# Performance work log

Measured on AMD Instinct MI355X. Metric: run time of the kernel, lower is better.

## Reference

```python
import jax, jax.numpy as jnp
import numpy as np

V = 28996  # BERT_VOCAB_SIZE
D = 768    # input_size (BERT embedding dim)
H = 768    # hidden_size
B, T, S = 32, 48, 128


def setup_inputs() -> dict:
    key = jax.random.key(0)
    ks = jax.random.split(key, 10)
    w = lambda k, shape: jax.random.normal(k, shape, jnp.float32) * 0.02
    return {
        "x": jax.random.normal(ks[0], (B, T, D), jnp.float32),
        "hidden_state": jax.random.normal(ks[1], (B, H), jnp.float32),
        "encoder_attention": jax.random.normal(ks[2], (B, S, H), jnp.float32),
        # GRUCell params (torch layout: weight_ih (3H, D), weight_hh (3H, H))
        "W_ih": w(ks[3], (3 * H, D)), "W_hh": w(ks[4], (3 * H, H)),
        "b_ih": jnp.zeros((3 * H,), jnp.float32), "b_hh": jnp.zeros((3 * H,), jnp.float32),
        # prediction_layer
        "W_pred": w(ks[5], (V, H)), "b_pred": jnp.zeros((V,), jnp.float32),
        # decoder_att_linear
        "W_att": w(ks[6], (H, H)), "b_att": jnp.zeros((H,), jnp.float32),
        # decoder_attn_weighted_ctx
        "W_ctx": w(ks[7], (H, 2 * H)), "b_ctx": jnp.zeros((H,), jnp.float32),
    }


def reference(x, hidden_state, encoder_attention,
              W_ih, W_hh, b_ih, b_hh,
              W_pred, b_pred, W_att, b_att, W_ctx, b_ctx):
    def gru(xt, h):  # torch nn.GRUCell math
        gi = xt @ W_ih.T + b_ih  # (B, 3H)
        gh = h @ W_hh.T + b_hh
        i_r, i_z, i_n = jnp.split(gi, 3, axis=-1)
        h_r, h_z, h_n = jnp.split(gh, 3, axis=-1)
        r = jax.nn.sigmoid(i_r + h_r)
        z = jax.nn.sigmoid(i_z + h_z)
        n = jnp.tanh(i_n + r * h_n)
        return (1.0 - z) * n + z * h

    def step(h, xt):  # xt: (B, D)
        h = gru(xt, h)
        logits = h @ W_pred.T + b_pred                      # (B, V)
        a = h @ W_att.T + b_att                              # (B, H)
        scores = jax.nn.softmax(
            jnp.einsum('bh,bsh->bs', a, encoder_attention), axis=-1)
        ctx = jnp.einsum('bs,bsh->bh', scores, encoder_attention)
        h_new = jnp.tanh(jnp.concatenate([ctx, h], axis=-1) @ W_ctx.T + b_ctx)
        return h_new, logits

    xT = jnp.swapaxes(x, 0, 1)  # (T, B, D)
    _, logits = jax.lax.scan(step, hidden_state, xT)  # logits: (T, B, V)
    return jnp.swapaxes(logits, 0, 1)  # (B, T, V)
```

## Files before the change

kernel.cpp:

```cpp
#include <hip/hip_runtime.h>
#include <hip/hip_bf16.h>

using bf16 = __hip_bfloat16;

typedef __attribute__((ext_vector_type(8))) short short8;
typedef __attribute__((ext_vector_type(4))) float floatx4;

#define BB 32
#define TT 48
#define SS 128
#define HH 768
#define VV 28996

__device__ __forceinline__ float sigmoidf_(float x) { return 1.0f / (1.0f + expf(-x)); }
__device__ __forceinline__ float tanhf_(float x) {
    float xx = fminf(fmaxf(x, -15.0f), 15.0f);
    float e = expf(2.0f * xx);
    return (e - 1.0f) / (e + 1.0f);
}

__device__ __forceinline__ float ld1cg(const float* p) {
    return __hip_atomic_load((float*)p, __ATOMIC_RELAXED, __HIP_MEMORY_SCOPE_AGENT);
}
__device__ __forceinline__ float2 ld2cg(const float* p) {
    unsigned long long u = __hip_atomic_load((unsigned long long*)p,
                                             __ATOMIC_RELAXED, __HIP_MEMORY_SCOPE_AGENT);
    union { unsigned long long u; float2 f; } c; c.u = u; return c.f;
}
__device__ __forceinline__ void st1cg(float* p, float v) {
    __hip_atomic_store(p, v, __ATOMIC_RELAXED, __HIP_MEMORY_SCOPE_AGENT);
}

__device__ __forceinline__ void split1(float v, bf16& h, bf16& l) {
    h = (bf16)v;
    l = (bf16)(v - __bfloat162float(h));
}

#define XQ    294912
#define WIHQ  442368
#define EQ    786432
#define WC1Q  147456
#define WATS  589824

__global__ __launch_bounds__(256)
void split_ops(const float* __restrict__ x, const float* __restrict__ Wih,
               const float* __restrict__ E, const float* __restrict__ Wctx,
               const float* __restrict__ Watt,
               bf16* __restrict__ xh, bf16* __restrict__ xl,
               bf16* __restrict__ wihh, bf16* __restrict__ wihl,
               bf16* __restrict__ eh, bf16* __restrict__ el,
               bf16* __restrict__ wc1h, bf16* __restrict__ wc1l,
               bf16* __restrict__ wath, bf16* __restrict__ watl)
{
    int idx = blockIdx.x * 256 + threadIdx.x;
    if (idx < XQ + WIHQ + EQ) {
        const float* src; bf16 *dh, *dl; int off;
        if (idx < XQ)            { src = x;   dh = xh;   dl = xl;   off = idx; }
        else if (idx < XQ + WIHQ){ src = Wih; dh = wihh; dl = wihl; off = idx - XQ; }
        else                     { src = E;   dh = eh;   dl = el;   off = idx - XQ - WIHQ; }
        float4 v = ((const float4*)src)[off];
        union { bf16 b[4]; uint2 u; } oh, ol;
        split1(v.x, oh.b[0], ol.b[0]); split1(v.y, oh.b[1], ol.b[1]);
        split1(v.z, oh.b[2], ol.b[2]); split1(v.w, oh.b[3], ol.b[3]);
        ((uint2*)dh)[off] = oh.u; ((uint2*)dl)[off] = ol.u;
    } else if (idx < XQ + WIHQ + EQ + WC1Q) {
        int rem = idx - XQ - WIHQ - EQ;
        int j = rem / 192, c4 = rem - j * 192;
        float4 v = *(const float4*)(Wctx + (size_t)j * 1536 + 4 * c4);
        union { bf16 b[4]; uint2 u; } oh, ol;
        split1(v.x, oh.b[0], ol.b[0]); split1(v.y, oh.b[1], ol.b[1]);
        split1(v.z, oh.b[2], ol.b[2]); split1(v.w, oh.b[3], ol.b[3]);
        ((uint2*)wc1h)[rem] = oh.u; ((uint2*)wc1l)[rem] = ol.u;
    } else if (idx < XQ + WIHQ + EQ + WC1Q + WATS) {
        int rem = idx - XQ - WIHQ - EQ - WC1Q;
        int n = rem / 768, k = rem - n * 768;
        float v = Watt[(size_t)k * 768 + n];
        bf16 h, l; split1(v, h, l);
        wath[rem] = h; watl[rem] = l;
    }
}

__global__ __launch_bounds__(256)
void gbias_k(const float* __restrict__ E, const float* __restrict__ batt,
             float* __restrict__ gbias)
{
    int row = blockIdx.x * 4 + (threadIdx.x >> 6);
    int lane = threadIdx.x & 63;
    const float* er = E + (size_t)row * 768;
    float acc = 0.f;
#pragma unroll
    for (int i = 0; i < 12; ++i) acc += er[i * 64 + lane] * batt[i * 64 + lane];
#pragma unroll
    for (int d = 32; d > 0; d >>= 1) acc += __shfl_xor(acc, d);
    if (lane == 0) gbias[row] = acc;
}

#define WPQ 5567232
__global__ __launch_bounds__(256)
void conv_pred(const float* __restrict__ Wp, bf16* __restrict__ Wpb)
{
    int idx = blockIdx.x * 256 + threadIdx.x;
    if (idx >= WPQ) return;
    float4 v = ((const float4*)Wp)[idx];
    union { bf16 b[4]; uint2 u; } o;
    o.b[0] = (bf16)v.x; o.b[1] = (bf16)v.y; o.b[2] = (bf16)v.z; o.b[3] = (bf16)v.w;
    ((uint2*)Wpb)[idx] = o.u;
}

__global__ __launch_bounds__(256)
void gemm_split(const bf16* __restrict__ Ahi, const bf16* __restrict__ Alo, int lda,
                const bf16* __restrict__ Bhi, const bf16* __restrict__ Blo, int ldb,
                const float* __restrict__ bias,
                float* __restrict__ C, int ldc, int M, int N, int K)
{
    __shared__ __align__(16) char smem[65536];
    const int tid  = threadIdx.x;
    const int lane = tid & 63;
    const int widx = tid >> 6;
    const int wm = widx >> 1, wn = widx & 1;
    const int m0 = blockIdx.y * 128, n0 = blockIdx.x * 128;

    floatx4 acc[4][4];
    const floatx4 fzero = {0.f, 0.f, 0.f, 0.f};
#pragma unroll
    for (int i = 0; i < 4; ++i)
#pragma unroll
        for (int j = 0; j < 4; ++j) acc[i][j] = fzero;

    const int srow = tid >> 3, sslot = tid & 7;

    for (int kb = 0; kb < K; kb += 64) {
        __syncthreads();
        const bf16* mats[4] = {Ahi, Alo, Bhi, Blo};
#pragma unroll
        for (int mt = 0; mt < 4; ++mt) {
            const bf16* base = mats[mt];
            int ld   = (mt < 2) ? lda : ldb;
            int row0 = (mt < 2) ? m0 : n0;
#pragma unroll
            for (int r = 0; r < 4; ++r) {
                int row = r * 32 + srow;
                int c = sslot ^ (row & 7);
                const bf16* gp = base + (size_t)(row0 + row) * ld + kb + c * 8;
                char* lp = smem + mt * 16384 + r * 4096 + widx * 1024;
                __builtin_amdgcn_global_load_lds(
                    (const __attribute__((address_space(1))) void*)gp,
                    (__attribute__((address_space(3))) void*)lp, 16, 0, 0);
            }
        }
        __syncthreads();
#pragma unroll
        for (int kc = 0; kc < 2; ++kc) {
            short8 ah[4], al[4], bh[4], bl[4];
#pragma unroll
            for (int i = 0; i < 4; ++i) {
                int mrow = wm * 64 + i * 16 + (lane & 15);
                int nrow = wn * 64 + i * 16 + (lane & 15);
                int ca = kc * 4 + (lane >> 4);
                int sm = (ca ^ (mrow & 7)) * 16, sn = (ca ^ (nrow & 7)) * 16;
                ah[i] = *(const short8*)(smem +         mrow * 128 + sm);
                al[i] = *(const short8*)(smem + 16384 + mrow * 128 + sm);
                bh[i] = *(const short8*)(smem + 32768 + nrow * 128 + sn);
                bl[i] = *(const short8*)(smem + 49152 + nrow * 128 + sn);
            }
#pragma unroll
            for (int i = 0; i < 4; ++i)
#pragma unroll
                for (int j = 0; j < 4; ++j) {
                    acc[i][j] = __builtin_amdgcn_mfma_f32_16x16x32_bf16(ah[i], bh[j], acc[i][j], 0, 0, 0);
                    acc[i][j] = __builtin_amdgcn_mfma_f32_16x16x32_bf16(ah[i], bl[j], acc[i][j], 0, 0, 0);
                    acc[i][j] = __builtin_amdgcn_mfma_f32_16x16x32_bf16(al[i], bh[j], acc[i][j], 0, 0, 0);
                }
        }
    }
#pragma unroll
    for (int i = 0; i < 4; ++i) {
        int gm0 = m0 + wm * 64 + i * 16 + (lane >> 4) * 4;
#pragma unroll
        for (int j = 0; j < 4; ++j) {
            int gn = n0 + wn * 64 + j * 16 + (lane & 15);
            float bv = bias ? bias[gn] : 0.0f;
#pragma unroll
            for (int r2 = 0; r2 < 4; ++r2)
                C[(size_t)(gm0 + r2) * ldc + gn] = acc[i][j][r2] + bv;
        }
    }
}

__global__ __launch_bounds__(256)
void gemm_bt(const bf16* __restrict__ A, int lda,
             const bf16* __restrict__ Bm, int ldb,
             const float* __restrict__ bias,
             float* __restrict__ C, int ldc, int M, int N, int K)
{
    __shared__ __align__(16) char smem[32768];
    const int tid  = threadIdx.x;
    const int lane = tid & 63;
    const int widx = tid >> 6;
    const int wm = widx >> 1, wn = widx & 1;
    const int m0 = blockIdx.y * 128, n0 = blockIdx.x * 128;

    floatx4 acc[4][4];
    const floatx4 fzero = {0.f, 0.f, 0.f, 0.f};
#pragma unroll
    for (int i = 0; i < 4; ++i)
#pragma unroll
        for (int j = 0; j < 4; ++j) acc[i][j] = fzero;

    const int srow = tid >> 3, sslot = tid & 7;

    for (int kb = 0; kb < K; kb += 64) {
        __syncthreads();
#pragma unroll
        for (int r = 0; r < 4; ++r) {
            int mrow = r * 32 + srow;
            int c = sslot ^ (mrow & 7);
            const bf16* gp = A + (size_t)(m0 + mrow) * lda + kb + c * 8;
            char* lp = smem + r * 4096 + widx * 1024;
            __builtin_amdgcn_global_load_lds(
                (const __attribute__((address_space(1))) void*)gp,
                (__attribute__((address_space(3))) void*)lp, 16, 0, 0);
        }
#pragma unroll
        for (int r = 0; r < 4; ++r) {
            int nrow = r * 32 + srow;
            int gn = n0 + nrow; if (gn > N - 1) gn = N - 1;
            int c = sslot ^ (nrow & 7);
            const bf16* gp = Bm + (size_t)gn * ldb + kb + c * 8;
            char* lp = smem + 16384 + r * 4096 + widx * 1024;
            __builtin_amdgcn_global_load_lds(
                (const __attribute__((address_space(1))) void*)gp,
                (__attribute__((address_space(3))) void*)lp, 16, 0, 0);
        }
        __syncthreads();
#pragma unroll
        for (int kc = 0; kc < 2; ++kc) {
            short8 af[4], bfr[4];
#pragma unroll
            for (int i = 0; i < 4; ++i) {
                int mrow = wm * 64 + i * 16 + (lane & 15);
                int nrow = wn * 64 + i * 16 + (lane & 15);
                int ca = kc * 4 + (lane >> 4);
                af[i]  = *(const short8*)(smem +         mrow * 128 + ((ca ^ (mrow & 7)) * 16));
                bfr[i] = *(const short8*)(smem + 16384 + nrow * 128 + ((ca ^ (nrow & 7)) * 16));
            }
#pragma unroll
            for (int i = 0; i < 4; ++i)
#pragma unroll
                for (int j = 0; j < 4; ++j)
                    acc[i][j] = __builtin_amdgcn_mfma_f32_16x16x32_bf16(af[i], bfr[j], acc[i][j], 0, 0, 0);
        }
    }
#pragma unroll
    for (int i = 0; i < 4; ++i) {
        int gm0 = m0 + wm * 64 + i * 16 + (lane >> 4) * 4;
#pragma unroll
        for (int j = 0; j < 4; ++j) {
            int gn = n0 + wn * 64 + j * 16 + (lane & 15);
            if (gn < N) {
                float bv = bias ? bias[gn] : 0.0f;
#pragma unroll
                for (int r2 = 0; r2 < 4; ++r2)
                    C[(size_t)(gm0 + r2) * ldc + gn] = acc[i][j][r2] + bv;
            }
        }
    }
}

__global__ __launch_bounds__(256)
void transpose_f(const float* __restrict__ F, float* __restrict__ Ft)
{
    __shared__ float tile[32][33];
    int tx = threadIdx.x & 31, ty = threadIdx.x >> 5;
    int r0 = blockIdx.x << 5, j0 = blockIdx.y << 5;
#pragma unroll
    for (int i = 0; i < 4; ++i)
        tile[ty + 8 * i][tx] = F[(size_t)(r0 + ty + 8 * i) * 768 + j0 + tx];
    __syncthreads();
#pragma unroll
    for (int i = 0; i < 4; ++i)
        Ft[(size_t)(j0 + ty + 8 * i) * 4096 + r0 + tx] = tile[tx][ty + 8 * i];
}

#define NBLK 256
__device__ __forceinline__ void flag_barrier(unsigned int* flags, unsigned int target)
{
    __syncthreads();
    if (threadIdx.x == 0)
        __hip_atomic_store(&flags[blockIdx.x * 4], target,
                           __ATOMIC_RELAXED, __HIP_MEMORY_SCOPE_AGENT);
    if (threadIdx.x < NBLK) {
        while (__hip_atomic_load(&flags[threadIdx.x * 4], __ATOMIC_RELAXED,
                                 __HIP_MEMORY_SCOPE_AGENT) < target)
            __builtin_amdgcn_s_sleep(1);
    }
    __syncthreads();
}

__global__ __launch_bounds__(512)
void seq_coop(const float* __restrict__ gi,
              const float* __restrict__ G,
              const float* __restrict__ Ft,
              const float* __restrict__ gbias,
              const float* __restrict__ h0,
              const float* __restrict__ Whh,
              const float* __restrict__ Wctx,
              const float* __restrict__ bhh,
              const float* __restrict__ bctx,
              float* __restrict__ Ha,
              float* __restrict__ Hb,
              float* __restrict__ Sc,
              unsigned int* __restrict__ flags,
              bf16* __restrict__ Hseq)
{
    const int bid  = blockIdx.x;
    const int tid  = threadIdx.x;
    const int w    = tid >> 6;
    const int lane = tid & 63;
    const int kg   = lane & 7;
    const int bo   = lane >> 3;
    const int j0   = bid * 3;

    __shared__ __align__(16) float Wlds[12][768];
    __shared__ float part[8][9][32];
    __shared__ float redsum[9][32];
    __shared__ float c2s[3][32];
    __shared__ float pT[128][33];
    __shared__ float ctxp[3][4][32];

    for (int idx = tid; idx < 12 * 768; idx += 512) {
        int rr = idx / 768, k = idx - rr * 768;
        float v;
        if (rr < 9) {
            int gate = rr / 3, jj = rr - gate * 3;
            v = Whh[(size_t)(gate * 768 + j0 + jj) * 768 + k];
        } else {
            int jj = rr - 9;
            v = Wctx[(size_t)(j0 + jj) * 1536 + 768 + k];
        }
        (&Wlds[0][0])[idx] = v;
    }

    float bhr = 0.f, bhz = 0.f, bhn = 0.f, bcv = 0.f;
    if (tid < 96) {
        int jj = tid >> 5;
        bhr = bhh[j0 + jj]; bhz = bhh[768 + j0 + jj]; bhn = bhh[1536 + j0 + jj];
        bcv = bctx[j0 + jj];
    }
    const int bstar = bid >> 3;
    const int s0    = (bid & 7) * 16;
    const int k4b   = 3 * (8 * w + kg);

    unsigned int target = 1;
    __syncthreads();

#pragma unroll 1
    for (int t = 0; t < TT; ++t) {
        const float* hp = (t == 0) ? h0 : Ha;

        float e_ir = 0.f, e_iz = 0.f, e_inn = 0.f, e_hprev = 0.f;
        if (tid < 96) {
            int jj = tid >> 5, bb = tid & 31;
            const float* gir = gi + (size_t)(bb * TT + t) * 2304 + j0 + jj;
            e_ir = gir[0]; e_iz = gir[768]; e_inn = gir[1536];
            e_hprev = ld1cg(hp + bb * 768 + j0 + jj);
        }

        {
            float acc[9][4];
#pragma unroll
            for (int r = 0; r < 9; ++r)
#pragma unroll
                for (int q = 0; q < 4; ++q) acc[r][q] = 0.f;
            const float* hp_b = hp + bo * 768 + 4 * k4b;
            float2 h2[4][6];
#pragma unroll
            for (int q = 0; q < 4; ++q) {
                const float* hq = hp_b + q * 8 * 768;
#pragma unroll
                for (int i = 0; i < 6; ++i) h2[q][i] = ld2cg(hq + 2 * i);
            }
#pragma unroll
            for (int r = 0; r < 9; ++r) {
                const float* wr_ = &Wlds[r][4 * k4b];
#pragma unroll
                for (int i = 0; i < 6; ++i) {
                    float2 w2 = *(const float2*)(wr_ + 2 * i);
#pragma unroll
                    for (int q = 0; q < 4; ++q)
                        acc[r][q] += w2.x * h2[q][i].x + w2.y * h2[q][i].y;
                }
            }
#pragma unroll
            for (int r = 0; r < 9; ++r)
#pragma unroll
                for (int q = 0; q < 4; ++q) {
                    float v = acc[r][q];
                    v += __shfl_xor(v, 1); v += __shfl_xor(v, 2); v += __shfl_xor(v, 4);
                    if (kg == 0) part[w][r][bo + 8 * q] = v;
                }
        }
        __syncthreads();
        if (tid < 288) {
            int rr = tid >> 5, bb = tid & 31;
            float s = 0.f;
#pragma unroll
            for (int ww = 0; ww < 8; ++ww) s += part[ww][rr][bb];
            redsum[rr][bb] = s;
        }
        __syncthreads();
        if (tid < 96) {
            int jj = tid >> 5, bb = tid & 31;
            float r = sigmoidf_(e_ir + redsum[jj][bb] + bhr);
            float z = sigmoidf_(e_iz + redsum[3 + jj][bb] + bhz);
            float n = tanhf_(e_inn + r * (redsum[6 + jj][bb] + bhn));
            float ht = (1.f - z) * n + z * e_hprev;
            st1cg(&Hb[bb * 768 + j0 + jj], ht);
            Hseq[(size_t)(bb * TT + t) * 768 + j0 + jj] = (bf16)ht;
        }
        flag_barrier(flags, target); ++target;

        {
            float a2[3][4];
#pragma unroll
            for (int c = 0; c < 3; ++c)
#pragma unroll
                for (int q = 0; q < 4; ++q) a2[c][q] = 0.f;
            const float* hb_b = Hb + bo * 768 + 4 * k4b;
            float2 h2[4][6];
#pragma unroll
            for (int q = 0; q < 4; ++q) {
                const float* hq = hb_b + q * 8 * 768;
#pragma unroll
                for (int i = 0; i < 6; ++i) h2[q][i] = ld2cg(hq + 2 * i);
            }
#pragma unroll
            for (int c = 0; c < 3; ++c) {
                const float* wr_ = &Wlds[9 + c][4 * k4b];
#pragma unroll
                for (int i = 0; i < 6; ++i) {
                    float2 w2 = *(const float2*)(wr_ + 2 * i);
#pragma unroll
                    for (int q = 0; q < 4; ++q)
                        a2[c][q] += w2.x * h2[q][i].x + w2.y * h2[q][i].y;
                }
            }
#pragma unroll
            for (int c = 0; c < 3; ++c)
#pragma unroll
                for (int q = 0; q < 4; ++q) {
                    float v = a2[c][q];
                    v += __shfl_xor(v, 1); v += __shfl_xor(v, 2); v += __shfl_xor(v, 4);
                    if (kg == 0) part[w][c][bo + 8 * q] = v;
                }
        }
        {
            const float* hb = Hb + bstar * 768;
            float2 a[6];
#pragma unroll
            for (int q = 0; q < 3; ++q) {
                a[2 * q]     = ld2cg(hb + 4 * (q * 64 + lane));
                a[2 * q + 1] = ld2cg(hb + 4 * (q * 64 + lane) + 2);
            }
#pragma unroll
            for (int ss = 0; ss < 2; ++ss) {
                const int s = s0 + 2 * w + ss;
                const float* grow = G + (size_t)(bstar * 128 + s) * 768;
                float sa = 0.f;
#pragma unroll
                for (int q = 0; q < 3; ++q) {
                    float4 g4 = *(const float4*)(grow + 4 * (q * 64 + lane));
                    sa += a[2 * q].x * g4.x + a[2 * q].y * g4.y
                        + a[2 * q + 1].x * g4.z + a[2 * q + 1].y * g4.w;
                }
#pragma unroll
                for (int d = 32; d > 0; d >>= 1) sa += __shfl_xor(sa, d);
                if (lane == 0)
                    st1cg(&Sc[bstar * 128 + s], sa + gbias[bstar * 128 + s]);
            }
        }
        flag_barrier(flags, target); ++target;

        if (tid < 96) {
            int jj = tid >> 5, bb = tid & 31;
            float s = 0.f;
#pragma unroll
            for (int ww = 0; ww < 8; ++ww) s += part[ww][jj][bb];
            c2s[jj][bb] = s;
        }
        {
#pragma unroll
            for (int q = 0; q < 4; ++q) {
                int bb = 4 * w + q;
                float v0 = ld1cg(&Sc[bb * 128 + lane]);
                float v1 = ld1cg(&Sc[bb * 128 + 64 + lane]);
                float m = fmaxf(v0, v1);
#pragma unroll
                for (int d = 32; d > 0; d >>= 1) m = fmaxf(m, __shfl_xor(m, d));
                float e0 = expf(v0 - m), e1 = expf(v1 - m);
                float sum = e0 + e1;
#pragma unroll
                for (int d = 32; d > 0; d >>= 1) sum += __shfl_xor(sum, d);
                float inv = 1.f / sum;
                pT[lane][bb] = e0 * inv;
                pT[64 + lane][bb] = e1 * inv;
            }
        }
        __syncthreads();
        if (tid < 384) {
            int jj = tid >> 7, rem = tid & 127, sh = rem >> 5, bb = rem & 31;
            const float* fr = Ft + (size_t)(j0 + jj) * 4096 + bb * 128 + 32 * sh;
            float ca = 0.f;
#pragma unroll
            for (int q = 0; q < 8; ++q) {
                float4 f4 = *(const float4*)(fr + 4 * q);
                int sb = 32 * sh + 4 * q;
                ca += f4.x * pT[sb][bb] + f4.y * pT[sb + 1][bb]
                    + f4.z * pT[sb + 2][bb] + f4.w * pT[sb + 3][bb];
            }
            ctxp[jj][sh][bb] = ca;
        }
        __syncthreads();
        if (tid < 96) {
            int jj = tid >> 5, bb = tid & 31;
            float ctx = ctxp[jj][0][bb] + ctxp[jj][1][bb]
                      + ctxp[jj][2][bb] + ctxp[jj][3][bb];
            float u = c2s[jj][bb] + ctx + bcv;
            st1cg(&Ha[bb * 768 + j0 + jj], tanhf_(u));
        }
        flag_barrier(flags, target); ++target;
    }
}

extern "C" void kernel_launch(void* const* d_in, const int* in_sizes, int n_in,
                              void* d_out, int out_size, void* d_ws, size_t ws_size,
                              hipStream_t stream)
{
    const float* x      = (const float*)d_in[0];
    const float* h0     = (const float*)d_in[1];
    const float* E      = (const float*)d_in[2];
    const float* W_ih   = (const float*)d_in[3];
    const float* W_hh   = (const float*)d_in[4];
    const float* b_ih   = (const float*)d_in[5];
    const float* b_hh   = (const float*)d_in[6];
    const float* W_pred = (const float*)d_in[7];
    const float* b_pred = (const float*)d_in[8];
    const float* W_att  = (const float*)d_in[9];
    const float* b_att  = (const float*)d_in[10];
    const float* W_ctx  = (const float*)d_in[11];
    const float* b_ctx  = (const float*)d_in[12];
    float* out = (float*)d_out;

    char* ws = (char*)d_ws;
    float* gi    = (float*)(ws);
    float* G     = (float*)(ws + 14155776);
    float* F     = (float*)(ws + 26738688);
    bf16*  xh    = (bf16*)(ws + 39321600);
    bf16*  xl    = (bf16*)(ws + 41680896);
    bf16*  wihh  = (bf16*)(ws + 44040192);
    bf16*  wihl  = (bf16*)(ws + 47579136);
    bf16*  eh    = (bf16*)(ws + 51118080);
    bf16*  el    = (bf16*)(ws + 57409536);
    bf16*  wath  = (bf16*)(ws + 63700992);
    bf16*  watl  = (bf16*)(ws + 64880640);
    bf16*  wc1h  = (bf16*)(ws + 66060288);
    bf16*  wc1l  = (bf16*)(ws + 67239936);
    bf16*  Hseq  = (bf16*)(ws + 68419584);
    float* gbias = (float*)(ws + 70778880);
    float* Ha    = (float*)(ws + 70795264);
    float* Hb    = (float*)(ws + 70893568);
    float* Sc    = (float*)(ws + 70991872);
    unsigned int* flags = (unsigned int*)(ws + 71008256);
    float* Ft    = (float*)(ws + 51118080);
    bf16*  Wpredb = (bf16*)(ws);

    hipMemsetAsync(flags, 0, NBLK * 16, stream);

    split_ops<<<8832, 256, 0, stream>>>(x, W_ih, E, W_ctx, W_att,
                                        xh, xl, wihh, wihl, eh, el,
                                        wc1h, wc1l, wath, watl);
    gbias_k<<<1024, 256, 0, stream>>>(E, b_att, gbias);

    gemm_split<<<dim3(18, 12), 256, 0, stream>>>(
        xh, xl, 768, wihh, wihl, 768, b_ih, gi, 2304, BB * TT, 2304, 768);
    gemm_split<<<dim3(6, 32), 256, 0, stream>>>(
        eh, el, 768, wath, watl, 768, nullptr, G, 768, BB * SS, 768, 768);
    gemm_split<<<dim3(6, 32), 256, 0, stream>>>(
        eh, el, 768, wc1h, wc1l, 768, nullptr, F, 768, BB * SS, 768, 768);
    transpose_f<<<dim3(128, 24), 256, 0, stream>>>(F, Ft);

    seq_coop<<<NBLK, 512, 0, stream>>>(gi, G, Ft, gbias, h0, W_hh, W_ctx,
                                       b_hh, b_ctx, Ha, Hb, Sc, flags, Hseq);

    conv_pred<<<21747, 256, 0, stream>>>(W_pred, Wpredb);
    gemm_bt<<<dim3(227, 12), 256, 0, stream>>>(
        Hseq, 768, Wpredb, 768, b_pred, out, VV, BB * TT, VV, 768);
}
```

Measured before the change: 2.089 ms.

## Interleave K access for coalescing, drop a reduction sync, prefetch Ft before barrier

Changes the per-lane K slicing of the recurrent matvecs so lanes read interleaved float2 chunks instead of contiguous 12-element runs. This coalesces global h loads and spreads LDS weight reads across banks. It also folds the 288-thread partial-sum reduction into the gate threads, removing a __syncthreads, and makes the score dot product use interleaved float2 loads. The Ft context rows are prefetched into registers before the grid barrier so their latency overlaps the barrier wait, at the cost of more register pressure.

```diff
diff --git a/kernel.cpp b/kernel.cpp
--- a/kernel.cpp
+++ b/kernel.cpp
@@ -323,8 +323,6 @@
 
     __shared__ __align__(16) float Wlds[12][768];
     __shared__ float part[8][9][32];
-    __shared__ float redsum[9][32];
-    __shared__ float c2s[3][32];
     __shared__ float pT[128][33];
     __shared__ float ctxp[3][4][32];
 
@@ -349,7 +347,7 @@
     }
     const int bstar = bid >> 3;
     const int s0    = (bid & 7) * 16;
-    const int k4b   = 3 * (8 * w + kg);
+    const int kseg  = w * 96 + 2 * kg;
 
     unsigned int target = 1;
     __syncthreads();
@@ -372,20 +370,20 @@
             for (int r = 0; r < 9; ++r)
 #pragma unroll
                 for (int q = 0; q < 4; ++q) acc[r][q] = 0.f;
-            const float* hp_b = hp + bo * 768 + 4 * k4b;
+            const float* hp_b = hp + bo * 768 + kseg;
             float2 h2[4][6];
 #pragma unroll
             for (int q = 0; q < 4; ++q) {
                 const float* hq = hp_b + q * 8 * 768;
 #pragma unroll
-                for (int i = 0; i < 6; ++i) h2[q][i] = ld2cg(hq + 2 * i);
+                for (int i = 0; i < 6; ++i) h2[q][i] = ld2cg(hq + 16 * i);
             }
 #pragma unroll
             for (int r = 0; r < 9; ++r) {
-                const float* wr_ = &Wlds[r][4 * k4b];
+                const float* wr_ = &Wlds[r][kseg];
 #pragma unroll
                 for (int i = 0; i < 6; ++i) {
-                    float2 w2 = *(const float2*)(wr_ + 2 * i);
+                    float2 w2 = *(const float2*)(wr_ + 16 * i);
 #pragma unroll
                     for (int q = 0; q < 4; ++q)
                         acc[r][q] += w2.x * h2[q][i].x + w2.y * h2[q][i].y;
@@ -401,19 +399,18 @@
                 }
         }
         __syncthreads();
-        if (tid < 288) {
-            int rr = tid >> 5, bb = tid & 31;
-            float s = 0.f;
-#pragma unroll
-            for (int ww = 0; ww < 8; ++ww) s += part[ww][rr][bb];
-            redsum[rr][bb] = s;
-        }
-        __syncthreads();
         if (tid < 96) {
             int jj = tid >> 5, bb = tid & 31;
-            float r = sigmoidf_(e_ir + redsum[jj][bb] + bhr);
-            float z = sigmoidf_(e_iz + redsum[3 + jj][bb] + bhz);
-            float n = tanhf_(e_inn + r * (redsum[6 + jj][bb] + bhn));
+            float sr = 0.f, sz = 0.f, sn = 0.f;
+#pragma unroll
+            for (int ww = 0; ww < 8; ++ww) {
+                sr += part[ww][jj][bb];
+                sz += part[ww][3 + jj][bb];
+                sn += part[ww][6 + jj][bb];
+            }
+            float r = sigmoidf_(e_ir + sr + bhr);
+            float z = sigmoidf_(e_iz + sz + bhz);
+            float n = tanhf_(e_inn + r * (sn + bhn));
             float ht = (1.f - z) * n + z * e_hprev;
             st1cg(&Hb[bb * 768 + j0 + jj], ht);
             Hseq[(size_t)(bb * TT + t) * 768 + j0 + jj] = (bf16)ht;
@@ -426,20 +423,20 @@
             for (int c = 0; c < 3; ++c)
 #pragma unroll
                 for (int q = 0; q < 4; ++q) a2[c][q] = 0.f;
-            const float* hb_b = Hb + bo * 768 + 4 * k4b;
+            const float* hb_b = Hb + bo * 768 + kseg;
             float2 h2[4][6];
 #pragma unroll
             for (int q = 0; q < 4; ++q) {
                 const float* hq = hb_b + q * 8 * 768;
 #pragma unroll
-                for (int i = 0; i < 6; ++i) h2[q][i] = ld2cg(hq + 2 * i);
+                for (int i = 0; i < 6; ++i) h2[q][i] = ld2cg(hq + 16 * i);
             }
 #pragma unroll
             for (int c = 0; c < 3; ++c) {
-                const float* wr_ = &Wlds[9 + c][4 * k4b];
+                const float* wr_ = &Wlds[9 + c][kseg];
 #pragma unroll
                 for (int i = 0; i < 6; ++i) {
-                    float2 w2 = *(const float2*)(wr_ + 2 * i);
+                    float2 w2 = *(const float2*)(wr_ + 16 * i);
 #pragma unroll
                     for (int q = 0; q < 4; ++q)
                         a2[c][q] += w2.x * h2[q][i].x + w2.y * h2[q][i].y;
@@ -455,23 +452,19 @@
                 }
         }
         {
-            const float* hb = Hb + bstar * 768;
+            const float* hb = Hb + bstar * 768 + 2 * lane;
             float2 a[6];
 #pragma unroll
-            for (int q = 0; q < 3; ++q) {
-                a[2 * q]     = ld2cg(hb + 4 * (q * 64 + lane));
-                a[2 * q + 1] = ld2cg(hb + 4 * (q * 64 + lane) + 2);
-            }
+            for (int q = 0; q < 6; ++q) a[q] = ld2cg(hb + 128 * q);
 #pragma unroll
             for (int ss = 0; ss < 2; ++ss) {
                 const int s = s0 + 2 * w + ss;
-                const float* grow = G + (size_t)(bstar * 128 + s) * 768;
+                const float* grow = G + (size_t)(bstar * 128 + s) * 768 + 2 * lane;
                 float sa = 0.f;
 #pragma unroll
-                for (int q = 0; q < 3; ++q) {
-                    float4 g4 = *(const float4*)(grow + 4 * (q * 64 + lane));
-                    sa += a[2 * q].x * g4.x + a[2 * q].y * g4.y
-                        + a[2 * q + 1].x * g4.z + a[2 * q + 1].y * g4.w;
+                for (int q = 0; q < 6; ++q) {
+                    float2 g2 = *(const float2*)(grow + 128 * q);
+                    sa += a[q].x * g2.x + a[q].y * g2.y;
                 }
 #pragma unroll
                 for (int d = 32; d > 0; d >>= 1) sa += __shfl_xor(sa, d);
@@ -479,14 +472,22 @@
                     st1cg(&Sc[bstar * 128 + s], sa + gbias[bstar * 128 + s]);
             }
         }
+        floatx4 fpre[8];
+        {
+            int pjj = tid >> 7, prem = tid & 127, psh = prem >> 5, pbb = prem & 31;
+            const float* fr = Ft + (size_t)(j0 + pjj) * 4096 + pbb * 128 + 32 * psh;
+            if (tid < 384) {
+#pragma unroll
+                for (int q = 0; q < 8; ++q) fpre[q] = *(const floatx4*)(fr + 4 * q);
+            }
+        }
         flag_barrier(flags, target); ++target;
 
+        float c2v = 0.f;
         if (tid < 96) {
-            int jj = tid >> 5, bb = tid & 31;
-            float s = 0.f;
-#pragma unroll
-            for (int ww = 0; ww < 8; ++ww) s += part[ww][jj][bb];
-            c2s[jj][bb] = s;
+            int jjc = tid >> 5, bbc = tid & 31;
+#pragma unroll
+            for (int ww = 0; ww < 8; ++ww) c2v += part[ww][jjc][bbc];
         }
         {
 #pragma unroll
@@ -509,14 +510,12 @@
         __syncthreads();
         if (tid < 384) {
             int jj = tid >> 7, rem = tid & 127, sh = rem >> 5, bb = rem & 31;
-            const float* fr = Ft + (size_t)(j0 + jj) * 4096 + bb * 128 + 32 * sh;
             float ca = 0.f;
 #pragma unroll
             for (int q = 0; q < 8; ++q) {
-                float4 f4 = *(const float4*)(fr + 4 * q);
                 int sb = 32 * sh + 4 * q;
-                ca += f4.x * pT[sb][bb] + f4.y * pT[sb + 1][bb]
-                    + f4.z * pT[sb + 2][bb] + f4.w * pT[sb + 3][bb];
+                ca += fpre[q][0] * pT[sb][bb] + fpre[q][1] * pT[sb + 1][bb]
+                    + fpre[q][2] * pT[sb + 2][bb] + fpre[q][3] * pT[sb + 3][bb];
             }
             ctxp[jj][sh][bb] = ca;
         }
@@ -525,7 +524,7 @@
             int jj = tid >> 5, bb = tid & 31;
             float ctx = ctxp[jj][0][bb] + ctxp[jj][1][bb]
                       + ctxp[jj][2][bb] + ctxp[jj][3][bb];
-            float u = c2s[jj][bb] + ctx + bcv;
+            float u = c2v + ctx + bcv;
             st1cg(&Ha[bb * 768 + j0 + jj], tanhf_(u));
         }
         flag_barrier(flags, target); ++target;
```

After: 2.167 ms. 1.04x slower.
